# Optimization experiments

Hardware: AMD Instinct MI355X
Metric: run time of the kernel (lower is better)

## Reference

```python
import jax, jax.numpy as jnp
import numpy as np


def setup_inputs() -> dict:
    key = jax.random.key(0)
    k1, k2, k3 = jax.random.split(key, 3)
    E, D, N = 1000000, 128, 100000
    msg = jax.random.normal(k1, (E, D), dtype=jnp.float32)
    index = jax.random.randint(k2, (E,), 0, N, dtype=jnp.int32)
    t = jax.random.randint(k3, (E,), 0, 1000000, dtype=jnp.int32)
    return {"msg": msg, "index": index, "t": t, "dim_size": N}


def reference(msg, index, t, dim_size):
    # max_t[n] = max time among events targeting node n
    max_t = jax.ops.segment_max(t, index, num_segments=dim_size)
    # positions of events achieving the per-node max time; -1 otherwise
    pos = jnp.arange(t.shape[0], dtype=jnp.int32)
    is_max = t == max_t[index]
    pos = jnp.where(is_max, pos, -1)
    # argmax[n] = last (highest-position) event index with max time, or <0 if node has no events
    argmax = jax.ops.segment_max(pos, index, num_segments=dim_size)
    valid = argmax >= 0
    gathered = msg[jnp.clip(argmax, 0)]  # [dim_size, D]
    return jnp.where(valid[:, None], gathered, jnp.zeros((), dtype=msg.dtype))
```

## Files before the change

### kernel.cpp

```cpp
#include <hip/hip_runtime.h>
#include <stdint.h>


__global__ void init_ws_kernel(unsigned long long* __restrict__ ws, int n) {
    int i = blockIdx.x * blockDim.x + threadIdx.x;
    if (i < n) ws[i] = 0ULL;
}

__global__ void scatter_max_kernel(const int* __restrict__ t,
                                   const int* __restrict__ idx,
                                   unsigned long long* __restrict__ ws,
                                   int E) {
    int i = blockIdx.x * blockDim.x + threadIdx.x;
    if (i >= E) return;
    unsigned long long key =
        ((unsigned long long)(unsigned int)t[i] << 32) | (unsigned int)(i + 1);
    unsigned long long* p = &ws[idx[i]];
    if (*p < key) {
        atomicMax(p, key);
    }
}

__global__ void gather_kernel(const unsigned long long* __restrict__ ws,
                              const float4* __restrict__ msg,
                              float4* __restrict__ out,
                              int N) {
    int gid = blockIdx.x * blockDim.x + threadIdx.x;
    int node = gid >> 5;
    int lane = gid & 31;
    if (node >= N) return;
    unsigned long long key = ws[node];
    float4 v = make_float4(0.f, 0.f, 0.f, 0.f);
    if (key != 0ULL) {
        int pos = (int)(unsigned int)(key & 0xFFFFFFFFULL) - 1;
        v = msg[(size_t)pos * 32 + lane];
    }
    out[(size_t)node * 32 + lane] = v;
}

extern "C" void kernel_launch(void* const* d_in, const int* in_sizes, int n_in,
                              void* d_out, int out_size, void* d_ws, size_t ws_size,
                              hipStream_t stream) {
    const float* msg = (const float*)d_in[0];
    const int* index = (const int*)d_in[1];
    const int* t     = (const int*)d_in[2];
    const int D = 128;
    const int E = in_sizes[0] / D;
    const int N = out_size / D;

    unsigned long long* ws = (unsigned long long*)d_ws;

    {
        int threads = 256;
        int blocks = (N + threads - 1) / threads;
        init_ws_kernel<<<blocks, threads, 0, stream>>>(ws, N);
    }
    {
        int threads = 256;
        int blocks = (E + threads - 1) / threads;
        scatter_max_kernel<<<blocks, threads, 0, stream>>>(t, index, ws, E);
    }
    {
        int threads = 256;
        long long total = (long long)N * 32;
        int blocks = (int)((total + threads - 1) / threads);
        gather_kernel<<<blocks, threads, 0, stream>>>(
            ws, (const float4*)msg, (float4*)d_out, N);
    }
}
```

Baseline: 616.8 us.

## Split scatter-max into high-time and low-time passes with vectorized loads

The scatter is split into two passes around a hardcoded threshold of 750000. The first pass does atomicMax only for events at or above it, so later low-time events can be filtered by a plain read before any atomic. Both passes load t and index as int4 and handle four events per thread, and the gather kernel now covers two nodes per thread to raise memory-level parallelism. The threshold is tuned to the uniform time distribution of the test inputs; the result stays correct for any input but the speedup depends on that distribution, and E must be 4-aligned for the vector loads.

```diff
diff --git a/kernel.cpp b/kernel.cpp
--- a/kernel.cpp
+++ b/kernel.cpp
@@ -1,41 +1,92 @@
 #include <hip/hip_runtime.h>
 #include <stdint.h>
 
+static __device__ __forceinline__ unsigned long long pack_key(int t, int pos) {
+    return ((unsigned long long)(unsigned int)t << 32) | (unsigned int)(pos + 1);
+}
+
+#define T_HI 750000
 
 __global__ void init_ws_kernel(unsigned long long* __restrict__ ws, int n) {
     int i = blockIdx.x * blockDim.x + threadIdx.x;
     if (i < n) ws[i] = 0ULL;
 }
 
-__global__ void scatter_max_kernel(const int* __restrict__ t,
-                                   const int* __restrict__ idx,
-                                   unsigned long long* __restrict__ ws,
-                                   int E) {
-    int i = blockIdx.x * blockDim.x + threadIdx.x;
-    if (i >= E) return;
-    unsigned long long key =
-        ((unsigned long long)(unsigned int)t[i] << 32) | (unsigned int)(i + 1);
-    unsigned long long* p = &ws[idx[i]];
-    if (*p < key) {
-        atomicMax(p, key);
+__global__ void __launch_bounds__(256)
+scatter_hi_kernel(const int* __restrict__ t, const int* __restrict__ idx,
+                  unsigned long long* __restrict__ ws, int E) {
+    int i0 = (blockIdx.x * blockDim.x + threadIdx.x) * 4;
+    if (i0 + 3 < E) {
+        int4 tv = *(const int4*)(t + i0);
+        int4 iv = *(const int4*)(idx + i0);
+        if (tv.x >= T_HI) atomicMax(&ws[iv.x], pack_key(tv.x, i0 + 0));
+        if (tv.y >= T_HI) atomicMax(&ws[iv.y], pack_key(tv.y, i0 + 1));
+        if (tv.z >= T_HI) atomicMax(&ws[iv.z], pack_key(tv.z, i0 + 2));
+        if (tv.w >= T_HI) atomicMax(&ws[iv.w], pack_key(tv.w, i0 + 3));
+    } else if (i0 < E) {
+        for (int i = i0; i < E; ++i)
+            if (t[i] >= T_HI) atomicMax(&ws[idx[i]], pack_key(t[i], i));
     }
 }
 
-__global__ void gather_kernel(const unsigned long long* __restrict__ ws,
-                              const float4* __restrict__ msg,
-                              float4* __restrict__ out,
-                              int N) {
+__global__ void __launch_bounds__(256)
+scatter_lo_kernel(const int* __restrict__ t, const int* __restrict__ idx,
+                  unsigned long long* __restrict__ ws, int E) {
+    int i0 = (blockIdx.x * blockDim.x + threadIdx.x) * 4;
+    if (i0 + 3 < E) {
+        int4 tv = *(const int4*)(t + i0);
+        int4 iv = *(const int4*)(idx + i0);
+        if (tv.x < T_HI) {
+            unsigned long long k = pack_key(tv.x, i0 + 0);
+            if (ws[iv.x] < k) atomicMax(&ws[iv.x], k);
+        }
+        if (tv.y < T_HI) {
+            unsigned long long k = pack_key(tv.y, i0 + 1);
+            if (ws[iv.y] < k) atomicMax(&ws[iv.y], k);
+        }
+        if (tv.z < T_HI) {
+            unsigned long long k = pack_key(tv.z, i0 + 2);
+            if (ws[iv.z] < k) atomicMax(&ws[iv.z], k);
+        }
+        if (tv.w < T_HI) {
+            unsigned long long k = pack_key(tv.w, i0 + 3);
+            if (ws[iv.w] < k) atomicMax(&ws[iv.w], k);
+        }
+    } else if (i0 < E) {
+        for (int i = i0; i < E; ++i) {
+            if (t[i] < T_HI) {
+                unsigned long long k = pack_key(t[i], i);
+                if (ws[idx[i]] < k) atomicMax(&ws[idx[i]], k);
+            }
+        }
+    }
+}
+
+__global__ void __launch_bounds__(256)
+gather_kernel(const unsigned long long* __restrict__ ws,
+              const float4* __restrict__ msg,
+              float4* __restrict__ out, int N, int half) {
     int gid = blockIdx.x * blockDim.x + threadIdx.x;
-    int node = gid >> 5;
     int lane = gid & 31;
-    if (node >= N) return;
-    unsigned long long key = ws[node];
-    float4 v = make_float4(0.f, 0.f, 0.f, 0.f);
-    if (key != 0ULL) {
-        int pos = (int)(unsigned int)(key & 0xFFFFFFFFULL) - 1;
-        v = msg[(size_t)pos * 32 + lane];
+    int na = gid >> 5;
+    if (na >= half) return;
+    int nb = na + half;
+
+    unsigned long long ka = ws[na];
+    unsigned long long kb = (nb < N) ? ws[nb] : 0ULL;
+
+    float4 va = make_float4(0.f, 0.f, 0.f, 0.f);
+    float4 vb = va;
+    if (ka != 0ULL) {
+        int pa = (int)(unsigned int)(ka & 0xFFFFFFFFULL) - 1;
+        va = msg[(size_t)pa * 32 + lane];
     }
-    out[(size_t)node * 32 + lane] = v;
+    if (kb != 0ULL) {
+        int pb = (int)(unsigned int)(kb & 0xFFFFFFFFULL) - 1;
+        vb = msg[(size_t)pb * 32 + lane];
+    }
+    out[(size_t)na * 32 + lane] = va;
+    if (nb < N) out[(size_t)nb * 32 + lane] = vb;
 }
 
 extern "C" void kernel_launch(void* const* d_in, const int* in_sizes, int n_in,
@@ -57,14 +108,17 @@
     }
     {
         int threads = 256;
-        int blocks = (E + threads - 1) / threads;
-        scatter_max_kernel<<<blocks, threads, 0, stream>>>(t, index, ws, E);
+        int nthreads = (E + 3) / 4;
+        int blocks = (nthreads + threads - 1) / threads;
+        scatter_hi_kernel<<<blocks, threads, 0, stream>>>(t, index, ws, E);
+        scatter_lo_kernel<<<blocks, threads, 0, stream>>>(t, index, ws, E);
     }
     {
         int threads = 256;
-        long long total = (long long)N * 32;
+        int half = (N + 1) / 2;
+        long long total = (long long)half * 32;
         int blocks = (int)((total + threads - 1) / threads);
         gather_kernel<<<blocks, threads, 0, stream>>>(
-            ws, (const float4*)msg, (float4*)d_out, N);
+            ws, (const float4*)msg, (float4*)d_out, N, half);
     }
 }
```

New measurement: 602.5 us. -2.3%, faster.
